# Performance work log

Hardware: AMD Instinct MI355X
Metric: run time of the kernel (lower is better)

The kernel has to match this reference:

```python
import jax, jax.numpy as jnp
import numpy as np

HIDDEN = 64
CHANNELS = [256, 256, 256]
SHAPES = [(4, 256, 128, 128), (4, 256, 64, 64), (4, 256, 32, 32)]


def setup_inputs() -> dict:
    key = jax.random.key(0)
    ks = jax.random.split(key, 16)
    d = {}
    for i, shp in enumerate(SHAPES):
        d[f"x{i}"] = jax.random.normal(ks[i], shp, dtype=jnp.float32)
    kidx = 3
    for i, c in enumerate(CHANNELS):
        # convs1: 1x1 conv c -> HIDDEN (stored as [c_in, c_out] matrix)
        d[f"W1_{i}"] = jax.random.normal(ks[kidx], (c, HIDDEN), dtype=jnp.float32) * (1.0 / np.sqrt(c)); kidx += 1
        d[f"b1_{i}"] = jnp.zeros((HIDDEN,), dtype=jnp.float32)
        # convs2: 1x1 conv (HIDDEN + HIDDEN//2) -> c
        cin2 = HIDDEN + HIDDEN // 2
        d[f"W2_{i}"] = jax.random.normal(ks[kidx], (cin2, c), dtype=jnp.float32) * (1.0 / np.sqrt(cin2)); kidx += 1
        d[f"b2_{i}"] = jnp.zeros((c,), dtype=jnp.float32)
    return d


def _conv1x1(x, W, b):
    # x: [B, Cin, H, W], W: [Cin, Cout] -> [B, Cout, H, W]
    return jnp.einsum("bchw,cd->bdhw", x, W) + b[None, :, None, None]


def _level(x, W1, b1, W2, b2):
    y = _conv1x1(x, W1, b1)                      # [B, HIDDEN, H, W]
    out, fmap = jnp.split(y, 2, axis=1)          # each [B, HIDDEN//2, H, W]
    z = jnp.concatenate([out, fmap, jax.nn.relu(fmap)], axis=1)  # [B, 1.5*HIDDEN, H, W]
    return _conv1x1(z, W2, b2)                   # [B, Cin, H, W]


def reference(x0, x1, x2,
              W1_0, b1_0, W2_0, b2_0,
              W1_1, b1_1, W2_1, b2_1,
              W1_2, b1_2, W2_2, b2_2):
    o0 = _level(x0, W1_0, b1_0, W2_0, b2_0)
    o1 = _level(x1, W1_1, b1_1, W2_1, b2_1)
    o2 = _level(x2, W1_2, b1_2, W2_2, b2_2)
    return (o0, o1, o2)
```

## Files before the change

kernel.cpp:

```cpp
#include <hip/hip_runtime.h>

typedef __attribute__((ext_vector_type(8))) short short8;
typedef __attribute__((ext_vector_type(4))) float float4v;

__device__ __forceinline__ unsigned short f2bf(float f) {
    unsigned u = __float_as_uint(f);
    u = (u + 0x7FFFu + ((u >> 16) & 1u)) >> 16;
    return (unsigned short)u;
}

#define XSET 520
#define CROW 68
#define SMEM_BYTES 34816

__global__ void prepack(const float* __restrict__ W1_0, const float* __restrict__ W2_0,
                        const float* __restrict__ W1_1, const float* __restrict__ W2_1,
                        const float* __restrict__ W1_2, const float* __restrict__ W2_2,
                        unsigned short* __restrict__ ws) {
    int e = blockIdx.x * 256 + threadIdx.x;
    if (e >= 3 * 40960) return;
    int l = e / 40960, r = e % 40960;
    const float* W1 = (l == 0) ? W1_0 : (l == 1) ? W1_1 : W1_2;
    const float* W2 = (l == 0) ? W2_0 : (l == 1) ? W2_1 : W2_2;
    unsigned short* base = ws + l * 40960;
    if (r < 16384) {
        int j = r & 7, lane = (r >> 3) & 63, fs = r >> 9;
        int mt = fs >> 3, ks = fs & 7;
        int k = ks * 32 + (lane >> 4) * 8 + j;
        int m = mt * 16 + (lane & 15);
        base[r] = f2bf(W1[k * 64 + m]);
    } else {
        int r2 = r - 16384;
        int j = r2 & 7, lane = (r2 >> 3) & 63, fs = r2 >> 9;
        int mt = fs / 3, ks = fs - mt * 3;
        int k = ks * 32 + (lane >> 4) * 8 + j;
        int m = mt * 16 + (lane & 15);
        base[16384 + r2] = f2bf(W2[k * 256 + m]);
    }
}

template<int HW>
__device__ __forceinline__ void level3(
    const float* __restrict__ x,
    const unsigned short* __restrict__ A1,
    const unsigned short* __restrict__ A2,
    const float* __restrict__ b1, const float* __restrict__ b2,
    float* __restrict__ o, int px0,
    unsigned short* __restrict__ xs)
{
    const int t = (int)threadIdx.x;
    const int lane = t & 63, w = t >> 6;
    const int q = lane >> 4, n = lane & 15;
    unsigned short* zs = xs;

    {
        const int ch_lo = t >> 4;
        const int pp = t & 15;
        const int g = pp >> 2;
        const int n0 = (pp & 3) * 4;
        const float* xp = x + (size_t)ch_lo * HW + px0 + 4 * pp;
        float4v v[16];
#pragma unroll
        for (int i = 0; i < 16; ++i)
            v[i] = *(const float4v*)(xp + (size_t)(i * 16) * HW);
#pragma unroll
        for (int i = 0; i < 16; ++i) {
            const int ch = i * 16 + ch_lo;
            const int ks = ch >> 5, qq = (ch >> 3) & 3, j = ch & 7;
            unsigned short* base = xs + (g * 8 + ks) * XSET + g * 8 + j;
#pragma unroll
            for (int e = 0; e < 4; ++e)
                base[(qq * 16 + n0 + e) * 8] = f2bf(v[i][e]);
        }
    }
    __syncthreads();

    float4v acc1[4];
#pragma unroll
    for (int mt = 0; mt < 4; ++mt)
        acc1[mt] = *(const float4v*)(b1 + mt * 16 + q * 4);

    short8 xf[8];
#pragma unroll
    for (int ks = 0; ks < 8; ++ks)
        xf[ks] = *(const short8*)(xs + (w * 8 + ks) * XSET + w * 8 + lane * 8);
    __syncthreads();

    const short8* A1f = (const short8*)A1;
#pragma unroll
    for (int ks = 0; ks < 8; ++ks)
#pragma unroll
        for (int mt = 0; mt < 4; ++mt)
            acc1[mt] = __builtin_amdgcn_mfma_f32_16x16x32_bf16(
                A1f[(mt * 8 + ks) * 64 + lane], xf[ks], acc1[mt], 0, 0, 0);

    {
        unsigned short* zg = zs + w * 3 * XSET;
#pragma unroll
        for (int mt = 0; mt < 4; ++mt) {
            const int kb = mt * 16 + q * 4;
            unsigned long long pk =
                  (unsigned long long)f2bf(acc1[mt][0])
                | ((unsigned long long)f2bf(acc1[mt][1]) << 16)
                | ((unsigned long long)f2bf(acc1[mt][2]) << 32)
                | ((unsigned long long)f2bf(acc1[mt][3]) << 48);
            *(unsigned long long*)(zg + (kb >> 5) * XSET +
                (((kb >> 3) & 3) * 16 + n) * 8 + (kb & 7)) = pk;
            if (mt >= 2) {
                const int kr = kb + 32;
                unsigned long long pr =
                      (unsigned long long)f2bf(fmaxf(acc1[mt][0], 0.f))
                    | ((unsigned long long)f2bf(fmaxf(acc1[mt][1], 0.f)) << 16)
                    | ((unsigned long long)f2bf(fmaxf(acc1[mt][2], 0.f)) << 32)
                    | ((unsigned long long)f2bf(fmaxf(acc1[mt][3], 0.f)) << 48);
                *(unsigned long long*)(zg + (kr >> 5) * XSET +
                    (((kr >> 3) & 3) * 16 + n) * 8 + (kr & 7)) = pr;
            }
        }
    }
    __syncthreads();

    float4v acc2[4][4];
#pragma unroll
    for (int mm = 0; mm < 4; ++mm) {
        float4v bb = *(const float4v*)(b2 + (w * 4 + mm) * 16 + q * 4);
#pragma unroll
        for (int g = 0; g < 4; ++g) acc2[mm][g] = bb;
    }

    const short8* A2f = (const short8*)A2;
#pragma unroll
    for (int g = 0; g < 4; ++g) {
        short8 zf[3];
#pragma unroll
        for (int ks = 0; ks < 3; ++ks)
            zf[ks] = *(const short8*)(zs + (g * 3 + ks) * XSET + lane * 8);
#pragma unroll
        for (int ks = 0; ks < 3; ++ks)
#pragma unroll
            for (int mm = 0; mm < 4; ++mm)
                acc2[mm][g] = __builtin_amdgcn_mfma_f32_16x16x32_bf16(
                    A2f[((w * 4 + mm) * 3 + ks) * 64 + lane], zf[ks], acc2[mm][g], 0, 0, 0);
    }
    __syncthreads();

    float* cw = (float*)xs + w * 32 * CROW;
#pragma unroll
    for (int p = 0; p < 2; ++p) {
#pragma unroll
        for (int mp = 0; mp < 2; ++mp) {
            const int mm = p * 2 + mp;
#pragma unroll
            for (int g = 0; g < 4; ++g)
#pragma unroll
                for (int r = 0; r < 4; ++r)
                    cw[(mp * 16 + q * 4 + r) * CROW + g * 16 + n] = acc2[mm][g][r];
        }
        const int chs = lane >> 4;
        const int pp = lane & 15;
        float* op = o + (size_t)(w * 64 + p * 32 + chs) * HW + px0 + 4 * pp;
#pragma unroll
        for (int i = 0; i < 8; ++i) {
            float4v v = *(const float4v*)(cw + (i * 4 + chs) * CROW + 4 * pp);
            *(float4v*)(op + (size_t)(i * 4) * HW) = v;
        }
    }
}

__global__ __launch_bounds__(256, 4) void fused_v6(
    const float* __restrict__ x0, const float* __restrict__ x1, const float* __restrict__ x2,
    const float* __restrict__ b1_0, const float* __restrict__ b2_0,
    const float* __restrict__ b1_1, const float* __restrict__ b2_1,
    const float* __restrict__ b1_2, const float* __restrict__ b2_2,
    const unsigned short* __restrict__ wpk, float* __restrict__ out)
{
    __shared__ __align__(16) unsigned char smem[SMEM_BYTES];
    unsigned short* xs = (unsigned short*)smem;
    const int bi = (int)blockIdx.x;

    if (bi < 1024) {
        int b = bi >> 8, px0 = (bi & 255) * 64;
        level3<16384>(x0 + (size_t)b * 256 * 16384, wpk, wpk + 16384, b1_0, b2_0,
                      out + (size_t)b * 256 * 16384, px0, xs);
    } else if (bi < 1280) {
        int r = bi - 1024, b = r >> 6, px0 = (r & 63) * 64;
        level3<4096>(x1 + (size_t)b * 256 * 4096, wpk + 40960, wpk + 40960 + 16384,
                     b1_1, b2_1, out + 16777216 + (size_t)b * 256 * 4096, px0, xs);
    } else {
        int r = bi - 1280, b = r >> 4, px0 = (r & 15) * 64;
        level3<1024>(x2 + (size_t)b * 256 * 1024, wpk + 81920, wpk + 81920 + 16384,
                     b1_2, b2_2, out + 20971520 + (size_t)b * 256 * 1024, px0, xs);
    }
}

extern "C" void kernel_launch(void* const* d_in, const int* in_sizes, int n_in,
                              void* d_out, int out_size, void* d_ws, size_t ws_size,
                              hipStream_t stream) {
    const float* x0   = (const float*)d_in[0];
    const float* x1   = (const float*)d_in[1];
    const float* x2   = (const float*)d_in[2];
    const float* W1_0 = (const float*)d_in[3];
    const float* b1_0 = (const float*)d_in[4];
    const float* W2_0 = (const float*)d_in[5];
    const float* b2_0 = (const float*)d_in[6];
    const float* W1_1 = (const float*)d_in[7];
    const float* b1_1 = (const float*)d_in[8];
    const float* W2_1 = (const float*)d_in[9];
    const float* b2_1 = (const float*)d_in[10];
    const float* W1_2 = (const float*)d_in[11];
    const float* b1_2 = (const float*)d_in[12];
    const float* W2_2 = (const float*)d_in[13];
    const float* b2_2 = (const float*)d_in[14];
    float* out = (float*)d_out;
    unsigned short* wpk = (unsigned short*)d_ws;

    prepack<<<dim3(480), dim3(256), 0, stream>>>(W1_0, W2_0, W1_1, W2_1, W1_2, W2_2, wpk);
    fused_v6<<<dim3(1344), dim3(256), 0, stream>>>(
        x0, x1, x2, b1_0, b2_0, b1_1, b2_1, b1_2, b2_2, wpk, out);
}
```

Baseline: 195.3 us.

## Double pixel tile per block to 128 pixels, halving grid size

Each block now handles 128 pixels instead of 64, so every wave runs two pixel groups in the first GEMM and eight groups in the second. Per-wave reuse of the loaded weight fragments doubles and the grid shrinks to 672 blocks. LDS use roughly doubles, registers per thread grow (32 float4 loads in flight, 32 accumulators), and launch bounds drop to 2 blocks per CU, which lowers occupancy and latency hiding for this memory-bound kernel.

```diff
diff --git a/kernel.cpp b/kernel.cpp
--- a/kernel.cpp
+++ b/kernel.cpp
@@ -10,8 +10,8 @@
 }
 
 #define XSET 520
-#define CROW 68
-#define SMEM_BYTES 34816
+#define CROW2 130
+#define SMEM_BYTES 66688
 
 __global__ void prepack(const float* __restrict__ W1_0, const float* __restrict__ W2_0,
                         const float* __restrict__ W1_1, const float* __restrict__ W2_1,
@@ -54,18 +54,18 @@
     unsigned short* zs = xs;
 
     {
-        const int ch_lo = t >> 4;
-        const int pp = t & 15;
-        const int g = pp >> 2;
-        const int n0 = (pp & 3) * 4;
-        const float* xp = x + (size_t)ch_lo * HW + px0 + 4 * pp;
-        float4v v[16];
-#pragma unroll
-        for (int i = 0; i < 16; ++i)
-            v[i] = *(const float4v*)(xp + (size_t)(i * 16) * HW);
-#pragma unroll
-        for (int i = 0; i < 16; ++i) {
-            const int ch = i * 16 + ch_lo;
+        const int pxq = t & 31;
+        const int rh  = t >> 5;
+        const int g = pxq >> 2;
+        const int n0 = (pxq & 3) * 4;
+        const float* xp = x + (size_t)rh * HW + px0 + 4 * pxq;
+        float4v v[32];
+#pragma unroll
+        for (int i = 0; i < 32; ++i)
+            v[i] = *(const float4v*)(xp + (size_t)(i * 8) * HW);
+#pragma unroll
+        for (int i = 0; i < 32; ++i) {
+            const int ch = rh + 8 * i;
             const int ks = ch >> 5, qq = (ch >> 3) & 3, j = ch & 7;
             unsigned short* base = xs + (g * 8 + ks) * XSET + g * 8 + j;
 #pragma unroll
@@ -75,44 +75,52 @@
     }
     __syncthreads();
 
-    float4v acc1[4];
-#pragma unroll
-    for (int mt = 0; mt < 4; ++mt)
-        acc1[mt] = *(const float4v*)(b1 + mt * 16 + q * 4);
-
-    short8 xf[8];
-#pragma unroll
-    for (int ks = 0; ks < 8; ++ks)
-        xf[ks] = *(const short8*)(xs + (w * 8 + ks) * XSET + w * 8 + lane * 8);
-    __syncthreads();
+    short8 xf[2][8];
+#pragma unroll
+    for (int u = 0; u < 2; ++u)
+#pragma unroll
+        for (int ks = 0; ks < 8; ++ks)
+            xf[u][ks] = *(const short8*)(xs + ((2 * w + u) * 8 + ks) * XSET
+                                            + (2 * w + u) * 8 + lane * 8);
+    __syncthreads();
+
+    float4v acc1[2][4];
+#pragma unroll
+    for (int u = 0; u < 2; ++u)
+#pragma unroll
+        for (int mt = 0; mt < 4; ++mt)
+            acc1[u][mt] = *(const float4v*)(b1 + mt * 16 + q * 4);
 
     const short8* A1f = (const short8*)A1;
 #pragma unroll
-    for (int ks = 0; ks < 8; ++ks)
-#pragma unroll
-        for (int mt = 0; mt < 4; ++mt)
-            acc1[mt] = __builtin_amdgcn_mfma_f32_16x16x32_bf16(
-                A1f[(mt * 8 + ks) * 64 + lane], xf[ks], acc1[mt], 0, 0, 0);
-
-    {
-        unsigned short* zg = zs + w * 3 * XSET;
+    for (int u = 0; u < 2; ++u)
+#pragma unroll
+        for (int ks = 0; ks < 8; ++ks)
+#pragma unroll
+            for (int mt = 0; mt < 4; ++mt)
+                acc1[u][mt] = __builtin_amdgcn_mfma_f32_16x16x32_bf16(
+                    A1f[(mt * 8 + ks) * 64 + lane], xf[u][ks], acc1[u][mt], 0, 0, 0);
+
+#pragma unroll
+    for (int u = 0; u < 2; ++u) {
+        unsigned short* zg = zs + (2 * w + u) * 3 * XSET;
 #pragma unroll
         for (int mt = 0; mt < 4; ++mt) {
             const int kb = mt * 16 + q * 4;
             unsigned long long pk =
-                  (unsigned long long)f2bf(acc1[mt][0])
-                | ((unsigned long long)f2bf(acc1[mt][1]) << 16)
-                | ((unsigned long long)f2bf(acc1[mt][2]) << 32)
-                | ((unsigned long long)f2bf(acc1[mt][3]) << 48);
+                  (unsigned long long)f2bf(acc1[u][mt][0])
+                | ((unsigned long long)f2bf(acc1[u][mt][1]) << 16)
+                | ((unsigned long long)f2bf(acc1[u][mt][2]) << 32)
+                | ((unsigned long long)f2bf(acc1[u][mt][3]) << 48);
             *(unsigned long long*)(zg + (kb >> 5) * XSET +
                 (((kb >> 3) & 3) * 16 + n) * 8 + (kb & 7)) = pk;
             if (mt >= 2) {
                 const int kr = kb + 32;
                 unsigned long long pr =
-                      (unsigned long long)f2bf(fmaxf(acc1[mt][0], 0.f))
-                    | ((unsigned long long)f2bf(fmaxf(acc1[mt][1], 0.f)) << 16)
-                    | ((unsigned long long)f2bf(fmaxf(acc1[mt][2], 0.f)) << 32)
-                    | ((unsigned long long)f2bf(fmaxf(acc1[mt][3], 0.f)) << 48);
+                      (unsigned long long)f2bf(fmaxf(acc1[u][mt][0], 0.f))
+                    | ((unsigned long long)f2bf(fmaxf(acc1[u][mt][1], 0.f)) << 16)
+                    | ((unsigned long long)f2bf(fmaxf(acc1[u][mt][2], 0.f)) << 32)
+                    | ((unsigned long long)f2bf(fmaxf(acc1[u][mt][3], 0.f)) << 48);
                 *(unsigned long long*)(zg + (kr >> 5) * XSET +
                     (((kr >> 3) & 3) * 16 + n) * 8 + (kr & 7)) = pr;
             }
@@ -120,17 +128,17 @@
     }
     __syncthreads();
 
-    float4v acc2[4][4];
+    float4v acc2[4][8];
 #pragma unroll
     for (int mm = 0; mm < 4; ++mm) {
         float4v bb = *(const float4v*)(b2 + (w * 4 + mm) * 16 + q * 4);
 #pragma unroll
-        for (int g = 0; g < 4; ++g) acc2[mm][g] = bb;
+        for (int g = 0; g < 8; ++g) acc2[mm][g] = bb;
     }
 
     const short8* A2f = (const short8*)A2;
 #pragma unroll
-    for (int g = 0; g < 4; ++g) {
+    for (int g = 0; g < 8; ++g) {
         short8 zf[3];
 #pragma unroll
         for (int ks = 0; ks < 3; ++ks)
@@ -144,30 +152,30 @@
     }
     __syncthreads();
 
-    float* cw = (float*)xs + w * 32 * CROW;
+    float* cw = (float*)xs + w * 32 * CROW2;
 #pragma unroll
     for (int p = 0; p < 2; ++p) {
 #pragma unroll
         for (int mp = 0; mp < 2; ++mp) {
             const int mm = p * 2 + mp;
 #pragma unroll
-            for (int g = 0; g < 4; ++g)
+            for (int g = 0; g < 8; ++g)
 #pragma unroll
                 for (int r = 0; r < 4; ++r)
-                    cw[(mp * 16 + q * 4 + r) * CROW + g * 16 + n] = acc2[mm][g][r];
-        }
-        const int chs = lane >> 4;
-        const int pp = lane & 15;
+                    cw[(mp * 16 + q * 4 + r) * CROW2 + g * 16 + n] = acc2[mm][g][r];
+        }
+        const int chs = lane >> 5;
+        const int pp = lane & 31;
         float* op = o + (size_t)(w * 64 + p * 32 + chs) * HW + px0 + 4 * pp;
 #pragma unroll
-        for (int i = 0; i < 8; ++i) {
-            float4v v = *(const float4v*)(cw + (i * 4 + chs) * CROW + 4 * pp);
-            *(float4v*)(op + (size_t)(i * 4) * HW) = v;
-        }
-    }
-}
-
-__global__ __launch_bounds__(256, 4) void fused_v6(
+        for (int i = 0; i < 16; ++i) {
+            float4v v = *(const float4v*)(cw + (2 * i + chs) * CROW2 + 4 * pp);
+            *(float4v*)(op + (size_t)(2 * i) * HW) = v;
+        }
+    }
+}
+
+__global__ __launch_bounds__(256, 2) void fused_v7(
     const float* __restrict__ x0, const float* __restrict__ x1, const float* __restrict__ x2,
     const float* __restrict__ b1_0, const float* __restrict__ b2_0,
     const float* __restrict__ b1_1, const float* __restrict__ b2_1,
@@ -178,18 +186,18 @@
     unsigned short* xs = (unsigned short*)smem;
     const int bi = (int)blockIdx.x;
 
-    if (bi < 1024) {
-        int b = bi >> 8, px0 = (bi & 255) * 64;
-        level3<16384>(x0 + (size_t)b * 256 * 16384, wpk, wpk + 16384, b1_0, b2_0,
-                      out + (size_t)b * 256 * 16384, px0, xs);
-    } else if (bi < 1280) {
-        int r = bi - 1024, b = r >> 6, px0 = (r & 63) * 64;
-        level3<4096>(x1 + (size_t)b * 256 * 4096, wpk + 40960, wpk + 40960 + 16384,
-                     b1_1, b2_1, out + 16777216 + (size_t)b * 256 * 4096, px0, xs);
+    if (bi < 512) {
+        int b = bi >> 7, px0 = (bi & 127) * 128;
+        level3<16384>(x0 + (size_t)b * 4194304, wpk, wpk + 16384, b1_0, b2_0,
+                      out + (size_t)b * 4194304, px0, xs);
+    } else if (bi < 640) {
+        int r = bi - 512, b = r >> 5, px0 = (r & 31) * 128;
+        level3<4096>(x1 + (size_t)b * 1048576, wpk + 40960, wpk + 57344,
+                     b1_1, b2_1, out + 16777216 + (size_t)b * 1048576, px0, xs);
     } else {
-        int r = bi - 1280, b = r >> 4, px0 = (r & 15) * 64;
-        level3<1024>(x2 + (size_t)b * 256 * 1024, wpk + 81920, wpk + 81920 + 16384,
-                     b1_2, b2_2, out + 20971520 + (size_t)b * 256 * 1024, px0, xs);
+        int r = bi - 640, b = r >> 3, px0 = (r & 7) * 128;
+        level3<1024>(x2 + (size_t)b * 262144, wpk + 81920, wpk + 98304,
+                     b1_2, b2_2, out + 20971520 + (size_t)b * 262144, px0, xs);
     }
 }
 
@@ -215,6 +223,6 @@
     unsigned short* wpk = (unsigned short*)d_ws;
 
     prepack<<<dim3(480), dim3(256), 0, stream>>>(W1_0, W2_0, W1_1, W2_1, W1_2, W2_2, wpk);
-    fused_v6<<<dim3(1344), dim3(256), 0, stream>>>(
+    fused_v7<<<dim3(672), dim3(256), 0, stream>>>(
         x0, x1, x2, b1_0, b2_0, b1_1, b2_1, b1_2, b2_2, wpk, out);
 }
```

After: 191.8 us. About the same (-1.8%).

## Process two pixel tiles per block, prefetching second tile during first compute

Applied to the files above, without the earlier changes.

Each block now handles two consecutive 64-pixel tiles. The global loads for the second tile are issued into registers before the first tile's MFMA work runs, so memory latency overlaps with compute. The grid is halved to 672 blocks and the launch bound is lowered to 3 blocks per SM to make room for the extra 16 float4 registers. The trade-off is lower occupancy and fewer blocks to spread across CUs on a bandwidth-bound kernel.

```diff
diff --git a/kernel.cpp b/kernel.cpp
--- a/kernel.cpp
+++ b/kernel.cpp
@@ -39,54 +39,33 @@
     }
 }
 
+__device__ __forceinline__ void scatter_x(const float4v v[16], unsigned short* xs,
+                                          int g, int n0, int ch_lo) {
+#pragma unroll
+    for (int i = 0; i < 16; ++i) {
+        const int ch = i * 16 + ch_lo;
+        const int ks = ch >> 5, qq = (ch >> 3) & 3, j = ch & 7;
+        unsigned short* base = xs + (g * 8 + ks) * XSET + g * 8 + j;
+#pragma unroll
+        for (int e = 0; e < 4; ++e)
+            base[(qq * 16 + n0 + e) * 8] = f2bf(v[i][e]);
+    }
+}
+
 template<int HW>
-__device__ __forceinline__ void level3(
-    const float* __restrict__ x,
-    const unsigned short* __restrict__ A1,
-    const unsigned short* __restrict__ A2,
+__device__ __forceinline__ void tile_body(
+    const short8 xf[8], const short8* __restrict__ A1f, const short8* __restrict__ A2f,
     const float* __restrict__ b1, const float* __restrict__ b2,
-    float* __restrict__ o, int px0,
-    unsigned short* __restrict__ xs)
+    float* __restrict__ o, int px0, unsigned short* __restrict__ xs,
+    int lane, int w, int q, int n)
 {
-    const int t = (int)threadIdx.x;
-    const int lane = t & 63, w = t >> 6;
-    const int q = lane >> 4, n = lane & 15;
     unsigned short* zs = xs;
-
-    {
-        const int ch_lo = t >> 4;
-        const int pp = t & 15;
-        const int g = pp >> 2;
-        const int n0 = (pp & 3) * 4;
-        const float* xp = x + (size_t)ch_lo * HW + px0 + 4 * pp;
-        float4v v[16];
-#pragma unroll
-        for (int i = 0; i < 16; ++i)
-            v[i] = *(const float4v*)(xp + (size_t)(i * 16) * HW);
-#pragma unroll
-        for (int i = 0; i < 16; ++i) {
-            const int ch = i * 16 + ch_lo;
-            const int ks = ch >> 5, qq = (ch >> 3) & 3, j = ch & 7;
-            unsigned short* base = xs + (g * 8 + ks) * XSET + g * 8 + j;
-#pragma unroll
-            for (int e = 0; e < 4; ++e)
-                base[(qq * 16 + n0 + e) * 8] = f2bf(v[i][e]);
-        }
-    }
-    __syncthreads();
 
     float4v acc1[4];
 #pragma unroll
     for (int mt = 0; mt < 4; ++mt)
         acc1[mt] = *(const float4v*)(b1 + mt * 16 + q * 4);
 
-    short8 xf[8];
-#pragma unroll
-    for (int ks = 0; ks < 8; ++ks)
-        xf[ks] = *(const short8*)(xs + (w * 8 + ks) * XSET + w * 8 + lane * 8);
-    __syncthreads();
-
-    const short8* A1f = (const short8*)A1;
 #pragma unroll
     for (int ks = 0; ks < 8; ++ks)
 #pragma unroll
@@ -128,7 +107,6 @@
         for (int g = 0; g < 4; ++g) acc2[mm][g] = bb;
     }
 
-    const short8* A2f = (const short8*)A2;
 #pragma unroll
     for (int g = 0; g < 4; ++g) {
         short8 zf[3];
@@ -161,13 +139,64 @@
         float* op = o + (size_t)(w * 64 + p * 32 + chs) * HW + px0 + 4 * pp;
 #pragma unroll
         for (int i = 0; i < 8; ++i) {
-            float4v v = *(const float4v*)(cw + (i * 4 + chs) * CROW + 4 * pp);
-            *(float4v*)(op + (size_t)(i * 4) * HW) = v;
+            float4v vv = *(const float4v*)(cw + (i * 4 + chs) * CROW + 4 * pp);
+            *(float4v*)(op + (size_t)(i * 4) * HW) = vv;
         }
     }
 }
 
-__global__ __launch_bounds__(256, 4) void fused_v6(
+template<int HW>
+__device__ __forceinline__ void level3_pair(
+    const float* __restrict__ x,
+    const unsigned short* __restrict__ A1,
+    const unsigned short* __restrict__ A2,
+    const float* __restrict__ b1, const float* __restrict__ b2,
+    float* __restrict__ o, int px0,
+    unsigned short* __restrict__ xs)
+{
+    const int t = (int)threadIdx.x;
+    const int lane = t & 63, w = t >> 6;
+    const int q = lane >> 4, n = lane & 15;
+    const short8* A1f = (const short8*)A1;
+    const short8* A2f = (const short8*)A2;
+
+    const int ch_lo = t >> 4;
+    const int pp = t & 15;
+    const int g = pp >> 2;
+    const int n0 = (pp & 3) * 4;
+    const float* xp = x + (size_t)ch_lo * HW + px0 + 4 * pp;
+
+    float4v v[16];
+#pragma unroll
+    for (int i = 0; i < 16; ++i)
+        v[i] = *(const float4v*)(xp + (size_t)(i * 16) * HW);
+    scatter_x(v, xs, g, n0, ch_lo);
+    __syncthreads();
+
+    short8 xf[8];
+#pragma unroll
+    for (int ks = 0; ks < 8; ++ks)
+        xf[ks] = *(const short8*)(xs + (w * 8 + ks) * XSET + w * 8 + lane * 8);
+    __syncthreads();
+
+#pragma unroll
+    for (int i = 0; i < 16; ++i)
+        v[i] = *(const float4v*)(xp + 64 + (size_t)(i * 16) * HW);
+
+    tile_body<HW>(xf, A1f, A2f, b1, b2, o, px0, xs, lane, w, q, n);
+    __syncthreads();
+
+    scatter_x(v, xs, g, n0, ch_lo);
+    __syncthreads();
+#pragma unroll
+    for (int ks = 0; ks < 8; ++ks)
+        xf[ks] = *(const short8*)(xs + (w * 8 + ks) * XSET + w * 8 + lane * 8);
+    __syncthreads();
+
+    tile_body<HW>(xf, A1f, A2f, b1, b2, o, px0 + 64, xs, lane, w, q, n);
+}
+
+__global__ __launch_bounds__(256, 3) void fused_v8(
     const float* __restrict__ x0, const float* __restrict__ x1, const float* __restrict__ x2,
     const float* __restrict__ b1_0, const float* __restrict__ b2_0,
     const float* __restrict__ b1_1, const float* __restrict__ b2_1,
@@ -178,18 +207,18 @@
     unsigned short* xs = (unsigned short*)smem;
     const int bi = (int)blockIdx.x;
 
-    if (bi < 1024) {
-        int b = bi >> 8, px0 = (bi & 255) * 64;
-        level3<16384>(x0 + (size_t)b * 256 * 16384, wpk, wpk + 16384, b1_0, b2_0,
-                      out + (size_t)b * 256 * 16384, px0, xs);
-    } else if (bi < 1280) {
-        int r = bi - 1024, b = r >> 6, px0 = (r & 63) * 64;
-        level3<4096>(x1 + (size_t)b * 256 * 4096, wpk + 40960, wpk + 40960 + 16384,
-                     b1_1, b2_1, out + 16777216 + (size_t)b * 256 * 4096, px0, xs);
+    if (bi < 512) {
+        int b = bi >> 7, px0 = (bi & 127) * 128;
+        level3_pair<16384>(x0 + (size_t)b * 4194304, wpk, wpk + 16384, b1_0, b2_0,
+                           out + (size_t)b * 4194304, px0, xs);
+    } else if (bi < 640) {
+        int r = bi - 512, b = r >> 5, px0 = (r & 31) * 128;
+        level3_pair<4096>(x1 + (size_t)b * 1048576, wpk + 40960, wpk + 57344,
+                          b1_1, b2_1, out + 16777216 + (size_t)b * 1048576, px0, xs);
     } else {
-        int r = bi - 1280, b = r >> 4, px0 = (r & 15) * 64;
-        level3<1024>(x2 + (size_t)b * 256 * 1024, wpk + 81920, wpk + 81920 + 16384,
-                     b1_2, b2_2, out + 20971520 + (size_t)b * 256 * 1024, px0, xs);
+        int r = bi - 640, b = r >> 3, px0 = (r & 7) * 128;
+        level3_pair<1024>(x2 + (size_t)b * 262144, wpk + 81920, wpk + 98304,
+                          b1_2, b2_2, out + 20971520 + (size_t)b * 262144, px0, xs);
     }
 }
 
@@ -215,6 +244,6 @@
     unsigned short* wpk = (unsigned short*)d_ws;
 
     prepack<<<dim3(480), dim3(256), 0, stream>>>(W1_0, W2_0, W1_1, W2_1, W1_2, W2_2, wpk);
-    fused_v6<<<dim3(1344), dim3(256), 0, stream>>>(
+    fused_v8<<<dim3(672), dim3(256), 0, stream>>>(
         x0, x1, x2, b1_0, b2_0, b1_1, b2_1, b1_2, b2_2, wpk, out);
 }
```

Result: slower. 288.7 us (+47.9%).
